# Optimization experiments

Hardware: AMD Instinct MI355X
Metric: run time of the kernel (lower is better)

The kernel has to match this reference:

```python
import jax, jax.numpy as jnp
from jax import lax
import numpy as np

B, N, M, K = 16, 4096, 1024, 32
FEAT, H = 64, 128
GEO_IN = K * (3 + 2)      # 160: CGA embedding widens each row from 3 to 5
GEO_MID_IN = H + 2        # 130: CGA embedding appends (-1, -|x|^2/2) after hidden layer
FEAT_IN = K * FEAT        # 2048: vanilla MLP flattens the neighborhood


def setup_inputs() -> dict:
    key = jax.random.key(0)
    ks = jax.random.split(key, 8)
    def w(k, shape):
        return jax.random.normal(k, shape, jnp.float32) / np.float32(np.sqrt(shape[-1]))
    return {
        "xyz": jax.random.normal(ks[0], (B, N, 3), jnp.float32),
        "features": jax.random.normal(ks[1], (B, N, FEAT), jnp.float32),
        "geo_W1": w(ks[2], (H, GEO_IN)),
        "geo_Wout": w(ks[3], (H, GEO_MID_IN)),
        "feat_W1": w(ks[4], (H, FEAT_IN)),
        "feat_b1": jnp.zeros((H,), jnp.float32),
        "feat_Wout": w(ks[5], (H, H)),
        "feat_bout": jnp.zeros((H,), jnp.float32),
    }


def fps(xyz, m):
    """Deterministic farthest point sampling (start at index 0 per batch). xyz [B,N,3] -> idx [B,m]."""
    b, n, _ = xyz.shape
    def step(carry, _):
        dists, last = carry                                  # [B,N], [B]
        last_pt = jnp.take_along_axis(xyz, last[:, None, None], axis=1)  # [B,1,3]
        d = jnp.sum((xyz - last_pt) ** 2, axis=-1)           # [B,N]
        dists = jnp.minimum(dists, d)
        nxt = jnp.argmax(dists, axis=1).astype(jnp.int32)
        return (dists, nxt), last
    init = (jnp.full((b, n), jnp.finfo(xyz.dtype).max, xyz.dtype),
            jnp.zeros((b,), jnp.int32))
    _, idxs = lax.scan(step, init, None, length=m)           # [m,B]
    return idxs.T                                            # [B,m]


def knn_idx(xyz, centroids, k):
    """k nearest neighbors of each centroid among xyz. -> [B,M,k] int32."""
    x2 = jnp.sum(xyz * xyz, axis=-1)                         # [B,N]
    c2 = jnp.sum(centroids * centroids, axis=-1)             # [B,M]
    d = c2[:, :, None] + x2[:, None, :] - 2.0 * jnp.einsum('bmd,bnd->bmn', centroids, xyz)
    _, idx = lax.top_k(-d, k)                                # nearest-first, [B,M,k]
    return idx


def gather_pts(points, idx):
    """points [B,N,C], idx [B,...] -> [B,...,C]."""
    return jax.vmap(lambda p, i: p[i])(points, idx)


def cga_embed(x):
    """Append -1 and -|x|^2/2 along last axis."""
    ones = -jnp.ones(x.shape[:-1] + (1,), x.dtype)
    sq = -0.5 * jnp.sum(x * x, axis=-1, keepdims=True)
    return jnp.concatenate([x, ones, sq], axis=-1)


def geo_mlp(x, W1, Wout):
    # x [BM, K, 3]; version=1 PointCMLP, identity activation, no bias
    x = cga_embed(x)                                         # [BM,K,5]
    x = x.reshape(x.shape[0], -1)                            # [BM,5K]
    x = x @ W1.T                                             # [BM,H]
    x = cga_embed(x)                                         # [BM,H+2]
    return x @ Wout.T                                        # [BM,H]


def feat_mlp(x, W1, b1, Wout, bout):
    # x [BM, K, F]; version=0 PointCMLP, relu, bias
    x = x.reshape(x.shape[0], -1)                            # [BM,K*F]
    x = jax.nn.relu(x @ W1.T + b1)                           # [BM,H]
    return x @ Wout.T + bout                                 # [BM,H]


def reference(xyz, features, geo_W1, geo_Wout, feat_W1, feat_b1, feat_Wout, feat_bout):
    b = xyz.shape[0]
    idx = fps(xyz, M)                                        # [B,M]
    centroids = gather_pts(xyz, idx)                         # [B,M,3]
    group_idx = knn_idx(xyz, centroids, K)                   # [B,M,K]
    grouped_xyz = gather_pts(xyz, group_idx) - centroids[:, :, None, :]  # [B,M,K,3]
    x_geo = geo_mlp(grouped_xyz.reshape(b * M, K, 3), geo_W1, geo_Wout).reshape(b, M, -1)
    grouped_feat = gather_pts(features, group_idx)           # [B,M,K,FEAT]
    x_feat = feat_mlp(grouped_feat.reshape(b * M, K, FEAT), feat_W1, feat_b1, feat_Wout, feat_bout).reshape(b, M, -1)
    x = jnp.concatenate([x_geo, x_feat], axis=-1)            # [B,M,2H]
    return centroids, x
```

## Files before the change

### kernel.cpp

```cpp
#include <hip/hip_runtime.h>
#include <float.h>

#pragma clang fp contract(off)

#define B_ 16
#define N_ 4096
#define M_ 1024
#define K_ 32
#define FEAT_ 64
#define H_ 128
#define GEO_IN_ 160
#define GEO_MID_ 130
#define FEAT_IN_ 2048

typedef unsigned short u16t;
typedef float f32x2 __attribute__((ext_vector_type(2)));

#define DPP_STEP_MAX(ctrl) \
  t=(unsigned)__builtin_amdgcn_update_dpp((int)v,(int)v,(ctrl),0xf,0xf,false); \
  v=(t>v)?t:v;
#define DPP_STEP_MIN(ctrl) \
  t=(unsigned)__builtin_amdgcn_update_dpp((int)v,(int)v,(ctrl),0xf,0xf,false); \
  v=(t<v)?t:v;

__device__ __forceinline__ unsigned wave_max_u32(unsigned v){
  unsigned t;
  DPP_STEP_MAX(0x111) DPP_STEP_MAX(0x112) DPP_STEP_MAX(0x114) DPP_STEP_MAX(0x118)
  DPP_STEP_MAX(0x142) DPP_STEP_MAX(0x143)
  return (unsigned)__builtin_amdgcn_readlane((int)v,63);
}
__device__ __forceinline__ unsigned wave_min_u32(unsigned v){
  unsigned t;
  DPP_STEP_MIN(0x111) DPP_STEP_MIN(0x112) DPP_STEP_MIN(0x114) DPP_STEP_MIN(0x118)
  DPP_STEP_MIN(0x142) DPP_STEP_MIN(0x143)
  return (unsigned)__builtin_amdgcn_readlane((int)v,63);
}

__global__ __launch_bounds__(256) void fps_kernel(
    const float* __restrict__ xyz, float* __restrict__ outc)
{
  const int b = blockIdx.x, tid = threadIdx.x;
  const int wv = tid >> 6;
  const float* xb = xyz + (size_t)b * (N_*3);
  __shared__ __align__(16) float4 pl[N_];
  __shared__ unsigned long long kkey[2][4];
  __shared__ __align__(16) float4 kxyz[2][4];
  __shared__ float clist[M_][3];

  for (int i=tid; i<N_; i+=256)
    pl[i] = make_float4(xb[i*3], xb[i*3+1], xb[i*3+2], 0.f);
  float lx=xb[0], ly=xb[1], lz=xb[2];
  if (tid==0){ clist[0][0]=lx; clist[0][1]=ly; clist[0][2]=lz; }
  __syncthreads();

  f32x2 PX[8], PY[8], PZ[8], DD[8];
#pragma unroll
  for (int p=0;p<8;p++){
    float4 a = pl[tid + 256*p];
    float4 c = pl[tid + 256*(p+8)];
    PX[p] = (f32x2){a.x, c.x};
    PY[p] = (f32x2){a.y, c.y};
    PZ[p] = (f32x2){a.z, c.z};
    DD[p] = (f32x2){FLT_MAX, FLT_MAX};
  }

  for (int t=1;t<M_;t++){
    f32x2 lxv=(f32x2){lx,lx}, lyv=(f32x2){ly,ly}, lzv=(f32x2){lz,lz};
    f32x2 bd2=(f32x2){-FLT_MAX,-FLT_MAX};
    int bpx=0, bpy=0;
#pragma unroll
    for (int p=0;p<8;p++){
      f32x2 dx=PX[p]-lxv, dy=PY[p]-lyv, dz=PZ[p]-lzv;
      f32x2 m1=dx*dx, m2=dy*dy, m3=dz*dz;
      f32x2 s=(m1+m2)+m3;
      f32x2 nd=__builtin_elementwise_min(DD[p], s);
      DD[p]=nd;
      if (nd.x>bd2.x){ bd2.x=nd.x; bpx=p; }
      if (nd.y>bd2.y){ bd2.y=nd.y; bpy=p; }
    }
    bool ywin = (bd2.y > bd2.x);
    float bd = ywin ? bd2.y : bd2.x;
    int   bi = tid + 256*(ywin ? bpy+8 : bpx);
    float4 myc = pl[bi];
    unsigned db=__float_as_uint(bd);
    unsigned smax=wave_max_u32(db);
    unsigned cand=(db==smax)?(unsigned)bi:0x7FFFFFFFu;
    unsigned sbi=wave_min_u32(cand);
    if ((unsigned)tid==(sbi&255u)){
      kkey[t&1][wv]=((unsigned long long)smax<<32)|(unsigned)(0xFFFFFFFFu-sbi);
      kxyz[t&1][wv]=myc;
    }
    __syncthreads();
    const unsigned long long* kp=kkey[t&1];
    const float4* cp=kxyz[t&1];
    unsigned long long k0=kp[0],k1=kp[1],k2=kp[2],k3=kp[3];
    float4 c0=cp[0],c1=cp[1],c2=cp[2],c3=cp[3];
    if (k1>k0){ k0=k1; c0=c1; }
    if (k3>k2){ k2=k3; c2=c3; }
    if (k2>k0){ k0=k2; c0=c2; }
    lx=c0.x; ly=c0.y; lz=c0.z;
    if (tid==0){ clist[t][0]=lx; clist[t][1]=ly; clist[t][2]=lz; }
  }
  __syncthreads();
  for (int e=tid; e<M_; e+=256){
    size_t cb=((size_t)b*M_+(size_t)e)*3;
    outc[cb]=clist[e][0]; outc[cb+1]=clist[e][1]; outc[cb+2]=clist[e][2];
  }
}

__global__ __launch_bounds__(256) void knn_kernel(
    const float* __restrict__ xyz, const float* __restrict__ outc,
    u16t* __restrict__ gidx16)
{
  const int w = blockIdx.x*4 + (threadIdx.x>>6);
  const int lane = threadIdx.x & 63;
  const int b = w >> 10;
  const float* xb = xyz + (size_t)b*(N_*3);
  float cx=outc[(size_t)w*3], cy=outc[(size_t)w*3+1], cz=outc[(size_t)w*3+2];
  float c2=__fadd_rn(__fadd_rn(__fmul_rn(cx,cx),__fmul_rn(cy,cy)),__fmul_rn(cz,cz));

  float lv=FLT_MAX; int lj=0;
#pragma unroll
  for (int j=0;j<64;j++){
    int i = lane + 64*j;
    float xx=xb[i*3], xy=xb[i*3+1], xz=xb[i*3+2];
    float x2=__fadd_rn(__fadd_rn(__fmul_rn(xx,xx),__fmul_rn(xy,xy)),__fmul_rn(xz,xz));
    float dt=__fadd_rn(__fadd_rn(__fmul_rn(cx,xx),__fmul_rn(cy,xy)),__fmul_rn(cz,xz));
    float d=__fsub_rn(__fadd_rn(c2,x2),__fmul_rn(2.f,dt));
    if (d<lv){ lv=d; lj=j; }
  }
  unsigned long long cons = 0ull;
  const int wb = w*K_;
  for (int k=0;k<K_;k++){
    unsigned u=__float_as_uint(lv);
    u = (u&0x80000000u) ? ~u : (u|0x80000000u);
    unsigned smin=wave_min_u32(u);
    unsigned cand=(u==smin)?(unsigned)(lane+64*lj):0xFFFFFFFFu;
    unsigned widx=wave_min_u32(cand);
    if (lane==0) gidx16[wb+k]=(u16t)widx;
    int owner=(int)(widx & 63u);
    int slot =(int)(widx >> 6);
    if (lane==owner) cons |= (1ull<<(unsigned)slot);
    if (k==K_-1) break;
    unsigned clo=(unsigned)__builtin_amdgcn_readlane((int)(unsigned)cons, owner);
    unsigned chi=(unsigned)__builtin_amdgcn_readlane((int)(unsigned)(cons>>32), owner);
    unsigned long long ocons=((unsigned long long)chi<<32)|(unsigned long long)clo;
    int ip = owner + 64*lane;
    float xx=xb[ip*3], xy=xb[ip*3+1], xz=xb[ip*3+2];
    float x2=__fadd_rn(__fadd_rn(__fmul_rn(xx,xx),__fmul_rn(xy,xy)),__fmul_rn(xz,xz));
    float dt=__fadd_rn(__fadd_rn(__fmul_rn(cx,xx),__fmul_rn(cy,xy)),__fmul_rn(cz,xz));
    float d=__fsub_rn(__fadd_rn(c2,x2),__fmul_rn(2.f,dt));
    unsigned uj=__float_as_uint(d);
    uj=(uj&0x80000000u)?~uj:(uj|0x80000000u);
    if ((ocons>>(unsigned)lane)&1ull) uj=0xFFFFFFFFu;
    unsigned smin2=wave_min_u32(uj);
    unsigned cs=(uj==smin2)?(unsigned)lane:64u;
    unsigned sslot=wave_min_u32(cs);
    float dnew=__uint_as_float((unsigned)__builtin_amdgcn_readlane(__float_as_int(d),(int)sslot));
    if (lane==owner){ lv=dnew; lj=(int)sslot; }
  }
}

__global__ __launch_bounds__(256) void geofeat_kernel(
    const float* __restrict__ xyz, const float* __restrict__ outc,
    const u16t* __restrict__ gidx16,
    const float* __restrict__ gW1, const float* __restrict__ gWout,
    const float* __restrict__ feats,
    const float* __restrict__ fW1, const float* __restrict__ fb1,
    const float* __restrict__ fWout, const float* __restrict__ fbout,
    float* __restrict__ xout)
{
  __shared__ float smem[160*33 + 64*128 + 32];
  const int t=threadIdx.x;
  if (blockIdx.x < 512){
    float (*Es)[33]  = (float(*)[33])smem;
    float (*Hs)[33]  = (float(*)[33])smem;
    float (*Ws)[128] = (float(*)[128])(smem + 160*33);
    float* ssv = smem + 160*33 + 64*128;

    const int g0=blockIdx.x*32;
    for (int p=t; p<1024; p+=256){
      int g=p>>5, kk=p&31;
      int gg=g0+g, b=gg>>10;
      int idx=gidx16[gg*K_+kk];
      const float* pt = xyz + ((size_t)b*N_+(size_t)idx)*3;
      const float* cc = outc + (size_t)gg*3;
      float dx=__fsub_rn(pt[0],cc[0]);
      float dy=__fsub_rn(pt[1],cc[1]);
      float dz=__fsub_rn(pt[2],cc[2]);
      float sq=__fadd_rn(__fadd_rn(__fmul_rn(dx,dx),__fmul_rn(dy,dy)),__fmul_rn(dz,dz));
      int r=5*kk;
      Es[r][g]=dx; Es[r+1][g]=dy; Es[r+2][g]=dz;
      Es[r+3][g]=-1.f; Es[r+4][g]=__fmul_rn(-0.5f,sq);
    }
    const int gsub=t>>4, hsub=t&15, h0=hsub*8;
    const int hw=t>>1;
    float acc[2][8];
#pragma unroll
    for (int a=0;a<2;a++)
#pragma unroll
      for (int j=0;j<8;j++) acc[a][j]=0.f;
    __syncthreads();

    for (int c=0;c<3;c++){
      int i0=c*64;
      if (c<2){
        int fw0=(t&1)*32;
        const float* wr = gW1 + (size_t)hw*GEO_IN_ + i0 + fw0;
        float4 wv[8];
#pragma unroll
        for (int e=0;e<8;e++) wv[e]=((const float4*)wr)[e];
#pragma unroll
        for (int e=0;e<8;e++){
          Ws[fw0+4*e+0][hw]=wv[e].x;
          Ws[fw0+4*e+1][hw]=wv[e].y;
          Ws[fw0+4*e+2][hw]=wv[e].z;
          Ws[fw0+4*e+3][hw]=wv[e].w;
        }
      } else {
        int fw0=(t&1)*16;
        const float* wr = gW1 + (size_t)hw*GEO_IN_ + 128 + fw0;
        float4 wv[4];
#pragma unroll
        for (int e=0;e<4;e++) wv[e]=((const float4*)wr)[e];
#pragma unroll
        for (int e=0;e<4;e++){
          Ws[fw0+4*e+0][hw]=wv[e].x;
          Ws[fw0+4*e+1][hw]=wv[e].y;
          Ws[fw0+4*e+2][hw]=wv[e].z;
          Ws[fw0+4*e+3][hw]=wv[e].w;
        }
      }
      __syncthreads();
      int len=(c==2)?32:64;
      for (int k2=0;k2<len;k2++){
        float x0=Es[i0+k2][2*gsub], x1=Es[i0+k2][2*gsub+1];
        const float* wp=&Ws[k2][h0];
        float4 wa=*(const float4*)wp;
        float4 wb=*(const float4*)(wp+4);
        acc[0][0]=__builtin_fmaf(x0,wa.x,acc[0][0]);
        acc[0][1]=__builtin_fmaf(x0,wa.y,acc[0][1]);
        acc[0][2]=__builtin_fmaf(x0,wa.z,acc[0][2]);
        acc[0][3]=__builtin_fmaf(x0,wa.w,acc[0][3]);
        acc[0][4]=__builtin_fmaf(x0,wb.x,acc[0][4]);
        acc[0][5]=__builtin_fmaf(x0,wb.y,acc[0][5]);
        acc[0][6]=__builtin_fmaf(x0,wb.z,acc[0][6]);
        acc[0][7]=__builtin_fmaf(x0,wb.w,acc[0][7]);
        acc[1][0]=__builtin_fmaf(x1,wa.x,acc[1][0]);
        acc[1][1]=__builtin_fmaf(x1,wa.y,acc[1][1]);
        acc[1][2]=__builtin_fmaf(x1,wa.z,acc[1][2]);
        acc[1][3]=__builtin_fmaf(x1,wa.w,acc[1][3]);
        acc[1][4]=__builtin_fmaf(x1,wb.x,acc[1][4]);
        acc[1][5]=__builtin_fmaf(x1,wb.y,acc[1][5]);
        acc[1][6]=__builtin_fmaf(x1,wb.z,acc[1][6]);
        acc[1][7]=__builtin_fmaf(x1,wb.w,acc[1][7]);
      }
      __syncthreads();
    }
#pragma unroll
    for (int a=0;a<2;a++)
#pragma unroll
      for (int j=0;j<8;j++)
        Hs[h0+j][2*gsub+a]=acc[a][j];
    __syncthreads();
    if (t<32){
      float ss=0.f;
      for (int h=0;h<H_;h++){ float v=Hs[h][t]; ss=__builtin_fmaf(v,v,ss); }
      ssv[t]=__fmul_rn(-0.5f,ss);
    }
#pragma unroll
    for (int a=0;a<2;a++)
#pragma unroll
      for (int j=0;j<8;j++) acc[a][j]=0.f;
    for (int c=0;c<2;c++){
      int i0=c*64;
      int fw0=(t&1)*32;
      const float* wr = gWout + (size_t)hw*GEO_MID_ + i0 + fw0;
      float2 wv2[16];
#pragma unroll
      for (int e=0;e<16;e++) wv2[e]=((const float2*)wr)[e];
      __syncthreads();
#pragma unroll
      for (int e=0;e<16;e++){
        Ws[fw0+2*e+0][hw]=wv2[e].x;
        Ws[fw0+2*e+1][hw]=wv2[e].y;
      }
      __syncthreads();
      for (int k2=0;k2<64;k2++){
        float x0=Hs[i0+k2][2*gsub], x1=Hs[i0+k2][2*gsub+1];
        const float* wp=&Ws[k2][h0];
        float4 wa=*(const float4*)wp;
        float4 wb=*(const float4*)(wp+4);
        acc[0][0]=__builtin_fmaf(x0,wa.x,acc[0][0]);
        acc[0][1]=__builtin_fmaf(x0,wa.y,acc[0][1]);
        acc[0][2]=__builtin_fmaf(x0,wa.z,acc[0][2]);
        acc[0][3]=__builtin_fmaf(x0,wa.w,acc[0][3]);
        acc[0][4]=__builtin_fmaf(x0,wb.x,acc[0][4]);
        acc[0][5]=__builtin_fmaf(x0,wb.y,acc[0][5]);
        acc[0][6]=__builtin_fmaf(x0,wb.z,acc[0][6]);
        acc[0][7]=__builtin_fmaf(x0,wb.w,acc[0][7]);
        acc[1][0]=__builtin_fmaf(x1,wa.x,acc[1][0]);
        acc[1][1]=__builtin_fmaf(x1,wa.y,acc[1][1]);
        acc[1][2]=__builtin_fmaf(x1,wa.z,acc[1][2]);
        acc[1][3]=__builtin_fmaf(x1,wa.w,acc[1][3]);
        acc[1][4]=__builtin_fmaf(x1,wb.x,acc[1][4]);
        acc[1][5]=__builtin_fmaf(x1,wb.y,acc[1][5]);
        acc[1][6]=__builtin_fmaf(x1,wb.z,acc[1][6]);
        acc[1][7]=__builtin_fmaf(x1,wb.w,acc[1][7]);
      }
    }
#pragma unroll
    for (int j=0;j<8;j++){
      int o=h0+j;
      float2 we=*(const float2*)(gWout + (size_t)o*GEO_MID_ + 128);
#pragma unroll
      for (int a=0;a<2;a++){
        float v=acc[a][j];
        v=__builtin_fmaf(-1.f, we.x, v);
        v=__builtin_fmaf(ssv[2*gsub+a], we.y, v);
        xout[(size_t)(g0+2*gsub+a)*256 + o]=v;
      }
    }
  } else {
    float (*Xs)[68]  = (float(*)[68])smem;
    float (*Ws)[128] = (float(*)[128])(smem + 64*68);
    float (*Hs)[68]  = (float(*)[68])smem;
    float (*WoS)[128]= (float(*)[128])(smem + 128*68);
    const int g0=(blockIdx.x-512)*64;
    const int gsub=t>>4;
    const int h0=(t&15)*8;
    const int glx=t>>2, fq=(t&3)*16;
    const int hw=t>>1, fw0=(t&1)*32;
    const int fw1=(t&1)*16;
    const int gld=g0+glx, bld=gld>>10;
    float acc[4][8];
#pragma unroll
    for (int a=0;a<4;a++)
#pragma unroll
      for (int j=0;j<8;j++) acc[a][j]=0.f;

    for (int kk=0;kk<K_;kk++){
      int nidx=gidx16[gld*K_+kk];
      const float* fr=feats + ((size_t)bld*N_+(size_t)nidx)*FEAT_ + fq;
      float4 p[4];
#pragma unroll
      for (int e=0;e<4;e++) p[e]=((const float4*)fr)[e];
      const float* wr=fW1 + (size_t)hw*FEAT_IN_ + kk*64 + fw0;
      float4 wv[8];
#pragma unroll
      for (int e=0;e<8;e++) wv[e]=((const float4*)wr)[e];
#pragma unroll
      for (int e=0;e<4;e++){
        Xs[fq+4*e+0][glx]=p[e].x;
        Xs[fq+4*e+1][glx]=p[e].y;
        Xs[fq+4*e+2][glx]=p[e].z;
        Xs[fq+4*e+3][glx]=p[e].w;
      }
#pragma unroll
      for (int e=0;e<8;e++){
        Ws[fw0+4*e+0][hw]=wv[e].x;
        Ws[fw0+4*e+1][hw]=wv[e].y;
        Ws[fw0+4*e+2][hw]=wv[e].z;
        Ws[fw0+4*e+3][hw]=wv[e].w;
      }
      __syncthreads();
#pragma unroll 4
      for (int k2=0;k2<64;k2++){
        float4 xv=*(const float4*)&Xs[k2][4*gsub];
        const float* wp=&Ws[k2][h0];
        float4 wa=*(const float4*)wp;
        float4 wb=*(const float4*)(wp+4);
        float xr[4]={xv.x,xv.y,xv.z,xv.w};
        float wf[8]={wa.x,wa.y,wa.z,wa.w,wb.x,wb.y,wb.z,wb.w};
#pragma unroll
        for (int a=0;a<4;a++)
#pragma unroll
          for (int j=0;j<8;j++)
            acc[a][j]=__builtin_fmaf(xr[a],wf[j],acc[a][j]);
      }
      __syncthreads();
    }
#pragma unroll
    for (int j=0;j<8;j++){
      float bv=fb1[h0+j];
#pragma unroll
      for (int a=0;a<4;a++)
        Hs[h0+j][4*gsub+a]=fmaxf(__fadd_rn(acc[a][j],bv),0.f);
    }
    float ac2[4][8];
#pragma unroll
    for (int a=0;a<4;a++)
#pragma unroll
      for (int j=0;j<8;j++) ac2[a][j]=0.f;
    for (int c=0;c<4;c++){
      const float* wr2=fWout + (size_t)hw*H_ + c*32 + fw1;
      float4 w2[4];
#pragma unroll
      for (int e=0;e<4;e++) w2[e]=((const float4*)wr2)[e];
      __syncthreads();
#pragma unroll
      for (int e=0;e<4;e++){
        WoS[fw1+4*e+0][hw]=w2[e].x;
        WoS[fw1+4*e+1][hw]=w2[e].y;
        WoS[fw1+4*e+2][hw]=w2[e].z;
        WoS[fw1+4*e+3][hw]=w2[e].w;
      }
      __syncthreads();
#pragma unroll 4
      for (int k2=0;k2<32;k2++){
        float4 xv=*(const float4*)&Hs[c*32+k2][4*gsub];
        const float* wp=&WoS[k2][h0];
        float4 wa=*(const float4*)wp;
        float4 wb=*(const float4*)(wp+4);
        float xr[4]={xv.x,xv.y,xv.z,xv.w};
        float wf[8]={wa.x,wa.y,wa.z,wa.w,wb.x,wb.y,wb.z,wb.w};
#pragma unroll
        for (int a=0;a<4;a++)
#pragma unroll
          for (int j=0;j<8;j++)
            ac2[a][j]=__builtin_fmaf(xr[a],wf[j],ac2[a][j]);
      }
    }
#pragma unroll
    for (int j=0;j<8;j++){
      float bv=fbout[h0+j];
#pragma unroll
      for (int a=0;a<4;a++)
        xout[(size_t)(g0+4*gsub+a)*256+128+h0+j]=__fadd_rn(ac2[a][j],bv);
    }
  }
}

extern "C" void kernel_launch(void* const* d_in, const int* in_sizes, int n_in,
                              void* d_out, int out_size, void* d_ws, size_t ws_size,
                              hipStream_t stream) {
  const float* xyz  =(const float*)d_in[0];
  const float* feats=(const float*)d_in[1];
  const float* gW1  =(const float*)d_in[2];
  const float* gWout=(const float*)d_in[3];
  const float* fW1  =(const float*)d_in[4];
  const float* fb1  =(const float*)d_in[5];
  const float* fWout=(const float*)d_in[6];
  const float* fbout=(const float*)d_in[7];
  float* out=(float*)d_out;

  u16t* gidx16=(u16t*)d_ws;
  float* xout = out + (size_t)B_*M_*3;

  fps_kernel    <<<dim3(B_),        dim3(256), 0, stream>>>(xyz, out);
  knn_kernel    <<<dim3((B_*M_)/4), dim3(256), 0, stream>>>(xyz, out, gidx16);
  geofeat_kernel<<<dim3(768),       dim3(256), 0, stream>>>(
      xyz, out, gidx16, gW1, gWout, feats, fW1, fb1, fWout, fbout, xout);
}
```

Measured before the change: 1.076 ms.

## Use bf16 MFMA for feature MLP GEMMs instead of scalar FP32 FMA

Rewrites the feature-MLP branch of the fused kernel so both GEMMs (the gathered neighborhood times W1, and the hidden layer times Wout) run on 16x16x32 bf16 MFMA instructions. Gathered features and weights are converted to bf16 with round-to-nearest-even and staged in padded shared memory, with the accumulators held in f32x4 fragments. This targets the FP32 FMA throughput cost of the feature GEMM, which dominates that branch. The price is reduced precision from bf16 inputs and a new shared-memory layout.

```diff
diff --git a/kernel.cpp b/kernel.cpp
--- a/kernel.cpp
+++ b/kernel.cpp
@@ -15,6 +15,17 @@
 
 typedef unsigned short u16t;
 typedef float f32x2 __attribute__((ext_vector_type(2)));
+typedef short bf16x8 __attribute__((ext_vector_type(8)));
+typedef float f32x4 __attribute__((ext_vector_type(4)));
+
+__device__ __forceinline__ unsigned short f2bf(float f){
+  unsigned x = __float_as_uint(f);
+  unsigned r = x + 0x7FFFu + ((x>>16)&1u);
+  return (unsigned short)(r>>16);
+}
+__device__ __forceinline__ unsigned pkbf(float lo, float hi){
+  return (unsigned)f2bf(lo) | ((unsigned)f2bf(hi)<<16);
+}
 
 #define DPP_STEP_MAX(ctrl) \
   t=(unsigned)__builtin_amdgcn_update_dpp((int)v,(int)v,(ctrl),0xf,0xf,false); \
@@ -170,7 +181,7 @@
     const float* __restrict__ fWout, const float* __restrict__ fbout,
     float* __restrict__ xout)
 {
-  __shared__ float smem[160*33 + 64*128 + 32];
+  __shared__ __align__(16) float smem[160*33 + 64*128 + 32];
   const int t=threadIdx.x;
   if (blockIdx.x < 512){
     float (*Es)[33]  = (float(*)[33])smem;
@@ -322,111 +333,94 @@
       }
     }
   } else {
-    float (*Xs)[68]  = (float(*)[68])smem;
-    float (*Ws)[128] = (float(*)[128])(smem + 64*68);
-    float (*Hs)[68]  = (float(*)[68])smem;
-    float (*WoS)[128]= (float(*)[128])(smem + 128*68);
+    short* As  = (short*)smem;
+    short* Bs  = (short*)smem + 64*72;
+    short* H2  = (short*)smem;
+    short* W2s = (short*)smem + 64*136;
     const int g0=(blockIdx.x-512)*64;
-    const int gsub=t>>4;
-    const int h0=(t&15)*8;
-    const int glx=t>>2, fq=(t&3)*16;
-    const int hw=t>>1, fw0=(t&1)*32;
-    const int fw1=(t&1)*16;
-    const int gld=g0+glx, bld=gld>>10;
-    float acc[4][8];
-#pragma unroll
-    for (int a=0;a<4;a++)
-#pragma unroll
-      for (int j=0;j<8;j++) acc[a][j]=0.f;
-
-    for (int kk=0;kk<K_;kk++){
-      int nidx=gidx16[gld*K_+kk];
-      const float* fr=feats + ((size_t)bld*N_+(size_t)nidx)*FEAT_ + fq;
-      float4 p[4];
-#pragma unroll
-      for (int e=0;e<4;e++) p[e]=((const float4*)fr)[e];
-      const float* wr=fW1 + (size_t)hw*FEAT_IN_ + kk*64 + fw0;
-      float4 wv[8];
-#pragma unroll
-      for (int e=0;e<8;e++) wv[e]=((const float4*)wr)[e];
-#pragma unroll
-      for (int e=0;e<4;e++){
-        Xs[fq+4*e+0][glx]=p[e].x;
-        Xs[fq+4*e+1][glx]=p[e].y;
-        Xs[fq+4*e+2][glx]=p[e].z;
-        Xs[fq+4*e+3][glx]=p[e].w;
-      }
+    const int w = t>>6, l = t&63;
+    const int row16 = l&15, kg = l>>4;
+    f32x4 acc[8];
+#pragma unroll
+    for (int f=0; f<8; f++) acc[f] = (f32x4){0.f,0.f,0.f,0.f};
+
+    const int gl = t>>2, fq = (t&3)*16;
+    const int gg = g0+gl, bld2 = gg>>10;
+    const int hR = t>>1, kh = (t&1)*32;
+
+    for (int kk=0; kk<K_; kk++){
+      int nidx = gidx16[gg*K_+kk];
+      const float* fr = feats + ((size_t)bld2*N_+(size_t)nidx)*FEAT_ + fq;
+      float4 p0=((const float4*)fr)[0], p1=((const float4*)fr)[1],
+             p2=((const float4*)fr)[2], p3=((const float4*)fr)[3];
+      unsigned* aw = (unsigned*)(As + gl*72 + fq);
+      aw[0]=pkbf(p0.x,p0.y); aw[1]=pkbf(p0.z,p0.w);
+      aw[2]=pkbf(p1.x,p1.y); aw[3]=pkbf(p1.z,p1.w);
+      aw[4]=pkbf(p2.x,p2.y); aw[5]=pkbf(p2.z,p2.w);
+      aw[6]=pkbf(p3.x,p3.y); aw[7]=pkbf(p3.z,p3.w);
+      const float* wr = fW1 + (size_t)hR*FEAT_IN_ + kk*64 + kh;
+      unsigned* bw = (unsigned*)(Bs + hR*72 + kh);
 #pragma unroll
       for (int e=0;e<8;e++){
-        Ws[fw0+4*e+0][hw]=wv[e].x;
-        Ws[fw0+4*e+1][hw]=wv[e].y;
-        Ws[fw0+4*e+2][hw]=wv[e].z;
-        Ws[fw0+4*e+3][hw]=wv[e].w;
-      }
-      __syncthreads();
-#pragma unroll 4
-      for (int k2=0;k2<64;k2++){
-        float4 xv=*(const float4*)&Xs[k2][4*gsub];
-        const float* wp=&Ws[k2][h0];
-        float4 wa=*(const float4*)wp;
-        float4 wb=*(const float4*)(wp+4);
-        float xr[4]={xv.x,xv.y,xv.z,xv.w};
-        float wf[8]={wa.x,wa.y,wa.z,wa.w,wb.x,wb.y,wb.z,wb.w};
-#pragma unroll
-        for (int a=0;a<4;a++)
-#pragma unroll
-          for (int j=0;j<8;j++)
-            acc[a][j]=__builtin_fmaf(xr[a],wf[j],acc[a][j]);
-      }
-      __syncthreads();
-    }
-#pragma unroll
-    for (int j=0;j<8;j++){
-      float bv=fb1[h0+j];
-#pragma unroll
-      for (int a=0;a<4;a++)
-        Hs[h0+j][4*gsub+a]=fmaxf(__fadd_rn(acc[a][j],bv),0.f);
-    }
-    float ac2[4][8];
-#pragma unroll
-    for (int a=0;a<4;a++)
-#pragma unroll
-      for (int j=0;j<8;j++) ac2[a][j]=0.f;
-    for (int c=0;c<4;c++){
-      const float* wr2=fWout + (size_t)hw*H_ + c*32 + fw1;
-      float4 w2[4];
-#pragma unroll
-      for (int e=0;e<4;e++) w2[e]=((const float4*)wr2)[e];
-      __syncthreads();
-#pragma unroll
-      for (int e=0;e<4;e++){
-        WoS[fw1+4*e+0][hw]=w2[e].x;
-        WoS[fw1+4*e+1][hw]=w2[e].y;
-        WoS[fw1+4*e+2][hw]=w2[e].z;
-        WoS[fw1+4*e+3][hw]=w2[e].w;
-      }
-      __syncthreads();
-#pragma unroll 4
-      for (int k2=0;k2<32;k2++){
-        float4 xv=*(const float4*)&Hs[c*32+k2][4*gsub];
-        const float* wp=&WoS[k2][h0];
-        float4 wa=*(const float4*)wp;
-        float4 wb=*(const float4*)(wp+4);
-        float xr[4]={xv.x,xv.y,xv.z,xv.w};
-        float wf[8]={wa.x,wa.y,wa.z,wa.w,wb.x,wb.y,wb.z,wb.w};
-#pragma unroll
-        for (int a=0;a<4;a++)
-#pragma unroll
-          for (int j=0;j<8;j++)
-            ac2[a][j]=__builtin_fmaf(xr[a],wf[j],ac2[a][j]);
-      }
-    }
-#pragma unroll
-    for (int j=0;j<8;j++){
-      float bv=fbout[h0+j];
-#pragma unroll
-      for (int a=0;a<4;a++)
-        xout[(size_t)(g0+4*gsub+a)*256+128+h0+j]=__fadd_rn(ac2[a][j],bv);
+        float4 wv=((const float4*)wr)[e];
+        bw[2*e+0]=pkbf(wv.x,wv.y);
+        bw[2*e+1]=pkbf(wv.z,wv.w);
+      }
+      __syncthreads();
+      const short* Ar = As + (16*w + row16)*72;
+#pragma unroll
+      for (int s=0; s<2; s++){
+        bf16x8 af = *(const bf16x8*)(Ar + s*32 + kg*8);
+#pragma unroll
+        for (int f=0; f<8; f++){
+          bf16x8 bfr = *(const bf16x8*)(Bs + (f*16+row16)*72 + s*32 + kg*8);
+          acc[f] = __builtin_amdgcn_mfma_f32_16x16x32_bf16(af, bfr, acc[f], 0,0,0);
+        }
+      }
+      __syncthreads();
+    }
+#pragma unroll
+    for (int f=0; f<8; f++){
+      float bv = fb1[f*16 + row16];
+#pragma unroll
+      for (int r=0; r<4; r++){
+        float v = fmaxf(__fadd_rn(acc[f][r], bv), 0.f);
+        H2[(16*w + kg*4 + r)*136 + f*16 + row16] = (short)f2bf(v);
+      }
+    }
+    {
+      const int oR = t>>1, hh = (t&1)*64;
+      const float* w2r = fWout + (size_t)oR*H_ + hh;
+      unsigned* ww = (unsigned*)(W2s + oR*136 + hh);
+#pragma unroll
+      for (int e=0;e<16;e++){
+        float4 wv=((const float4*)w2r)[e];
+        ww[2*e+0]=pkbf(wv.x,wv.y);
+        ww[2*e+1]=pkbf(wv.z,wv.w);
+      }
+    }
+    __syncthreads();
+    f32x4 ac2[8];
+#pragma unroll
+    for (int f=0; f<8; f++) ac2[f] = (f32x4){0.f,0.f,0.f,0.f};
+    const short* A2r = H2 + (16*w + row16)*136;
+#pragma unroll
+    for (int s2=0; s2<4; s2++){
+      bf16x8 a2 = *(const bf16x8*)(A2r + s2*32 + kg*8);
+#pragma unroll
+      for (int f=0; f<8; f++){
+        bf16x8 b2 = *(const bf16x8*)(W2s + (f*16+row16)*136 + s2*32 + kg*8);
+        ac2[f] = __builtin_amdgcn_mfma_f32_16x16x32_bf16(a2, b2, ac2[f], 0,0,0);
+      }
+    }
+#pragma unroll
+    for (int f=0; f<8; f++){
+      float bo = fbout[f*16 + row16];
+#pragma unroll
+      for (int r=0; r<4; r++){
+        int g = g0 + 16*w + kg*4 + r;
+        xout[(size_t)g*256 + 128 + f*16 + row16] = __fadd_rn(ac2[f][r], bo);
+      }
     }
   }
 }
```

Result: faster. 984.4 us (-8.5%).
